# Kernel optimization log

Hardware: AMD Instinct MI355X
Metric: run time of the kernel (lower is better)

Reference implementation:

```python
import jax, jax.numpy as jnp
import numpy as np

D_MODEL = 512

def setup_inputs() -> dict:
    key = jax.random.key(0)
    k1, k2, k3 = jax.random.split(key, 3)
    B, N1, N2 = 16, 2048, 2048
    x1 = jax.random.normal(k1, (B, N1, D_MODEL), dtype=jnp.float32)
    x2 = jax.random.normal(k2, (B, N2, D_MODEL), dtype=jnp.float32)
    node_mask = jnp.ones((B, N1), dtype=jnp.bool_)
    # learned parameter: q_proj weight, stored torch-style [out, in]
    Wq = jax.random.normal(k3, (D_MODEL, D_MODEL), dtype=jnp.float32) * (1.0 / np.sqrt(D_MODEL))
    return {"x1": x1, "x2": x2, "node_mask": node_mask, "Wq": Wq}


def reference(x1, x2, node_mask, Wq):
    # Q = x1 @ Wq^T   (torch Linear with weight [out, in], no bias)
    Q = jnp.einsum('bnd,ed->bne', x1, Wq)            # [B, N1, 512]
    D = x2                                            # [B, N2, 512]
    # similarity matrix L = Q @ D^T
    L = jnp.einsum('bnd,bmd->bnm', Q, D)              # [B, N1, N2]
    # attention over document axis (dim=2)
    A_D = jax.nn.softmax(L, axis=2)                   # [B, N1, N2]
    # C_D = Q^T @ A_D -> transposed to [B, N2, 512]
    C_D = jnp.einsum('bnd,bnm->bmd', Q, A_D)          # [B, N2, 512]
    # attention over query axis (dim=1), then transposed: A_Q [B, N2, N1]
    A_Q = jnp.swapaxes(jax.nn.softmax(L, axis=1), 1, 2)
    # C_Q = D^T @ A_Q -> transposed to [B, N1, 512]
    C_Q = jnp.einsum('bmd,bmn->bnd', D, A_Q)          # [B, N1, 512]
    return (C_Q, C_D, A_D, A_Q)
```

## Files before the change

kernel.cpp:

```cpp
#include <hip/hip_runtime.h>

namespace {

constexpr int Bn = 16;
constexpr int Nn = 2048;
constexpr int Dn = 512;

typedef _Float16 h4 __attribute__((ext_vector_type(4)));
typedef _Float16 h8 __attribute__((ext_vector_type(8)));
typedef float    fx4 __attribute__((ext_vector_type(4)));

__device__ __forceinline__ void gld16(const _Float16* g, _Float16* l) {
  typedef const void __attribute__((address_space(1))) gvoid;
  typedef void __attribute__((address_space(3))) lvoid;
  __builtin_amdgcn_global_load_lds((gvoid*)g, (lvoid*)l, 16, 0, 0);
}

__device__ __forceinline__ void stage_gld(const _Float16* __restrict__ g, int ld,
    int r0, int k0, _Float16* __restrict__ lds, int t)
{
  #pragma unroll
  for (int i = 0; i < 2; ++i) {
    int chunk = i*256 + t;
    gld16(g + (long)(r0 + (chunk >> 2))*ld + k0 + (chunk & 3)*8, lds + chunk*8);
  }
}

__device__ __forceinline__ void load_f32(const float* __restrict__ g, int ld,
    int r0, int k0, int t, fx4* regs)
{
  #pragma unroll
  for (int rd = 0; rd < 4; ++rd)
    regs[rd] = *(const fx4*)(g + (long)(r0 + rd*32 + (t >> 3))*ld + k0 + (t & 7)*4);
}
template<int S>
__device__ __forceinline__ void write_cvt(const fx4* regs, _Float16* __restrict__ lds, int t)
{
  const int c = (t & 7)*4;
  #pragma unroll
  for (int rd = 0; rd < 4; ++rd) {
    int r = rd*32 + (t >> 3);
    h4 o;
    #pragma unroll
    for (int i = 0; i < 4; ++i) o[i] = (_Float16)regs[rd][i];
    *(h4*)(lds + r*S + c) = o;
  }
}

struct RegsA3 { h8 v0, v1; fx4 k00, k01, k10, k11; };
__device__ __forceinline__ void load_A3(const _Float16* __restrict__ g, int ld,
    int r0, int k0, int t, const float* __restrict__ kofs, RegsA3& R)
{
  {
    int chunk = t, r = chunk >> 2, c = (chunk & 3)*8;
    R.v0  = *(const h8*)(g + (long)(r0 + r)*ld + k0 + c);
    R.k00 = *(const fx4*)(kofs + k0 + c);
    R.k01 = *(const fx4*)(kofs + k0 + c + 4);
  }
  {
    int chunk = 256 + t, r = chunk >> 2, c = (chunk & 3)*8;
    R.v1  = *(const h8*)(g + (long)(r0 + r)*ld + k0 + c);
    R.k10 = *(const fx4*)(kofs + k0 + c);
    R.k11 = *(const fx4*)(kofs + k0 + c + 4);
  }
}
template<int S>
__device__ __forceinline__ void write_A3(const RegsA3& R, _Float16* __restrict__ lds, int t)
{
  {
    int chunk = t, r = chunk >> 2, c = (chunk & 3)*8;
    h8 o;
    #pragma unroll
    for (int j = 0; j < 4; ++j) {
      o[j]   = (_Float16)__expf((float)R.v0[j]   - R.k00[j]);
      o[4+j] = (_Float16)__expf((float)R.v0[4+j] - R.k01[j]);
    }
    *(h8*)(lds + r*S + c) = o;
  }
  {
    int chunk = 256 + t, r = chunk >> 2, c = (chunk & 3)*8;
    h8 o;
    #pragma unroll
    for (int j = 0; j < 4; ++j) {
      o[j]   = (_Float16)__expf((float)R.v1[j]   - R.k10[j]);
      o[4+j] = (_Float16)__expf((float)R.v1[4+j] - R.k11[j]);
    }
    *(h8*)(lds + r*S + c) = o;
  }
}

template<int MA, int MB, int EPI, int TY>
__global__ __launch_bounds__(256) void gemm128(
    const void* __restrict__ Ap, long sA,
    const void* __restrict__ Bp, long sB,
    void* __restrict__ Cp, long sC, int ldc,
    void* __restrict__ C2p, long sC2, int ldc2,
    int lda, int ldb, int K,
    const float* __restrict__ kofs,
    float* __restrict__ rowPM, float* __restrict__ rowPS,
    float* __restrict__ colPM, float* __restrict__ colPS)
{
  constexpr int SA = (MA == 0) ? 32 : 40;
  constexpr int SB = (MB == 0) ? 32 : 40;
  constexpr int ASZ = 128*SA, BSZ = 128*SB;
  constexpr int DB = 2*ASZ + 2*BSZ;
  constexpr int SMEM = (EPI >= 1 && DB < 128*136) ? 128*136 : DB;
  __shared__ _Float16 smem[SMEM];

  constexpr int TILES = 16*TY;
  const int bid = blockIdx.x;
  const int xcd = bid & 7, slot = bid >> 3;
  const int b = xcd*2 + slot/TILES;
  const int tile = slot % TILES;
  const int by = tile % TY, bx = tile / TY;
  const int row0 = bx*128, col0 = by*128;

  const int t = threadIdx.x, w = t >> 6, l = t & 63;
  const int wr = w >> 1, wc = w & 1, l15 = l & 15, lg = l >> 4;

  const void* Ab;
  const void* Bb;
  if constexpr (MA == 1) Ab = (const void*)((const float*)Ap + (long)b*sA);
  else                   Ab = (const void*)((const _Float16*)Ap + (long)b*sA);
  if constexpr (MB == 1) Bb = (const void*)((const float*)Bp + (long)b*sB);
  else                   Bb = (const void*)((const _Float16*)Bp + (long)b*sB);

  const float* ko = nullptr;
  if constexpr (MA == 3) ko = kofs + (long)b*Nn;

  fx4 acc[4][4];
  #pragma unroll
  for (int fi = 0; fi < 4; ++fi)
    #pragma unroll
    for (int fj = 0; fj < 4; ++fj)
      acc[fi][fj] = (fx4){0.f, 0.f, 0.f, 0.f};

  const int NT = K/32;
  fx4 regA[4], regB[4];
  RegsA3 rA3;

  if constexpr (MA == 0)      stage_gld((const _Float16*)Ab, lda, row0, 0, smem, t);
  else if constexpr (MA == 1) load_f32((const float*)Ab, lda, row0, 0, t, regA);
  else                        load_A3((const _Float16*)Ab, lda, row0, 0, t, ko, rA3);
  if constexpr (MB == 0)      stage_gld((const _Float16*)Bb, ldb, col0, 0, smem + 2*ASZ, t);
  else                        load_f32((const float*)Bb, ldb, col0, 0, t, regB);
  if constexpr (MA == 1)      write_cvt<SA>(regA, smem, t);
  if constexpr (MA == 3)      write_A3<SA>(rA3, smem, t);
  if constexpr (MB == 1)      write_cvt<SB>(regB, smem + 2*ASZ, t);
  __syncthreads();

  for (int kt = 0; kt < NT; ++kt) {
    const int cur = kt & 1, nxt = cur ^ 1;
    const int k1 = (kt + 1)*32;
    _Float16* cA = smem + cur*ASZ;
    _Float16* cB = smem + 2*ASZ + cur*BSZ;
    _Float16* nA = smem + nxt*ASZ;
    _Float16* nB = smem + 2*ASZ + nxt*BSZ;

    if (kt + 1 < NT) {
      if constexpr (MA == 0)      stage_gld((const _Float16*)Ab, lda, row0, k1, nA, t);
      else if constexpr (MA == 1) load_f32((const float*)Ab, lda, row0, k1, t, regA);
      else                        load_A3((const _Float16*)Ab, lda, row0, k1, t, ko, rA3);
      if constexpr (MB == 0)      stage_gld((const _Float16*)Bb, ldb, col0, k1, nB, t);
      else                        load_f32((const float*)Bb, ldb, col0, k1, t, regB);
    }

    h8 af[4], bf[4];
    #pragma unroll
    for (int fi = 0; fi < 4; ++fi)
      af[fi] = *(const h8*)(cA + (wr*64 + fi*16 + l15)*SA + lg*8);
    #pragma unroll
    for (int fj = 0; fj < 4; ++fj)
      bf[fj] = *(const h8*)(cB + (wc*64 + fj*16 + l15)*SB + lg*8);
    #pragma unroll
    for (int fi = 0; fi < 4; ++fi)
      #pragma unroll
      for (int fj = 0; fj < 4; ++fj)
        acc[fi][fj] = __builtin_amdgcn_mfma_f32_16x16x32_f16(af[fi], bf[fj], acc[fi][fj], 0, 0, 0);

    if (kt + 1 < NT) {
      if constexpr (MA == 1) write_cvt<SA>(regA, nA, t);
      if constexpr (MA == 3) write_A3<SA>(rA3, nA, t);
      if constexpr (MB == 1) write_cvt<SB>(regB, nB, t);
    }
    __syncthreads();
  }

  if constexpr (EPI == 0) {
    float* Cb = (float*)Cp + (long)b*sC;
    #pragma unroll
    for (int fi = 0; fi < 4; ++fi)
      #pragma unroll
      for (int fj = 0; fj < 4; ++fj)
        #pragma unroll
        for (int j = 0; j < 4; ++j)
          Cb[(long)(row0 + wr*64 + fi*16 + lg*4 + j)*ldc + col0 + wc*64 + fj*16 + l15] = acc[fi][fj][j];
  }

  if constexpr (EPI == 1) {
    #pragma unroll
    for (int fi = 0; fi < 4; ++fi)
      #pragma unroll
      for (int fj = 0; fj < 4; ++fj)
        #pragma unroll
        for (int j = 0; j < 4; ++j)
          acc[fi][fj][j] = (float)(_Float16)acc[fi][fj][j];

    #pragma unroll
    for (int fi = 0; fi < 4; ++fi)
      #pragma unroll
      for (int fj = 0; fj < 4; ++fj)
        #pragma unroll
        for (int j = 0; j < 4; ++j)
          smem[(wr*64 + fi*16 + lg*4 + j)*136 + wc*64 + fj*16 + l15] = (_Float16)acc[fi][fj][j];
    __syncthreads();
    _Float16* Cb = (_Float16*)Cp + (long)b*sC;
    #pragma unroll
    for (int rd = 0; rd < 8; ++rd) {
      int r = rd*16 + (t >> 4), c8 = (t & 15)*8;
      h8 v = *(const h8*)(smem + r*136 + c8);
      *(h8*)(Cb + (long)(row0 + r)*ldc + col0 + c8) = v;
    }

    float rm[4][4], rs[4][4];
    #pragma unroll
    for (int fi = 0; fi < 4; ++fi)
      #pragma unroll
      for (int j = 0; j < 4; ++j)
        rm[fi][j] = fmaxf(fmaxf(acc[fi][0][j], acc[fi][1][j]),
                          fmaxf(acc[fi][2][j], acc[fi][3][j]));
    #pragma unroll
    for (int m = 1; m < 16; m <<= 1)
      #pragma unroll
      for (int fi = 0; fi < 4; ++fi)
        #pragma unroll
        for (int j = 0; j < 4; ++j)
          rm[fi][j] = fmaxf(rm[fi][j], __shfl_xor(rm[fi][j], m, 64));
    #pragma unroll
    for (int fi = 0; fi < 4; ++fi)
      #pragma unroll
      for (int j = 0; j < 4; ++j) {
        float s = 0.f;
        #pragma unroll
        for (int fj = 0; fj < 4; ++fj)
          s += __expf(acc[fi][fj][j] - rm[fi][j]);
        rs[fi][j] = s;
      }
    #pragma unroll
    for (int m = 1; m < 16; m <<= 1)
      #pragma unroll
      for (int fi = 0; fi < 4; ++fi)
        #pragma unroll
        for (int j = 0; j < 4; ++j)
          rs[fi][j] += __shfl_xor(rs[fi][j], m, 64);
    if (l15 == 0) {
      #pragma unroll
      for (int fi = 0; fi < 4; ++fi)
        #pragma unroll
        for (int j = 0; j < 4; ++j) {
          int row = row0 + wr*64 + fi*16 + lg*4 + j;
          long idx = ((long)b*Nn + row)*32 + by*2 + wc;
          rowPM[idx] = rm[fi][j];
          rowPS[idx] = rs[fi][j];
        }
    }
    float cm[4], cs[4];
    #pragma unroll
    for (int fj = 0; fj < 4; ++fj) {
      float v = -3.4e38f;
      #pragma unroll
      for (int fi = 0; fi < 4; ++fi)
        #pragma unroll
        for (int j = 0; j < 4; ++j)
          v = fmaxf(v, acc[fi][fj][j]);
      cm[fj] = v;
    }
    #pragma unroll
    for (int fj = 0; fj < 4; ++fj) {
      cm[fj] = fmaxf(cm[fj], __shfl_xor(cm[fj], 16, 64));
      cm[fj] = fmaxf(cm[fj], __shfl_xor(cm[fj], 32, 64));
    }
    #pragma unroll
    for (int fj = 0; fj < 4; ++fj) {
      float s = 0.f;
      #pragma unroll
      for (int fi = 0; fi < 4; ++fi)
        #pragma unroll
        for (int j = 0; j < 4; ++j)
          s += __expf(acc[fi][fj][j] - cm[fj]);
      cs[fj] = s;
    }
    #pragma unroll
    for (int fj = 0; fj < 4; ++fj) {
      cs[fj] += __shfl_xor(cs[fj], 16, 64);
      cs[fj] += __shfl_xor(cs[fj], 32, 64);
    }
    if (l < 16) {
      #pragma unroll
      for (int fj = 0; fj < 4; ++fj) {
        int col = col0 + wc*64 + fj*16 + l15;
        long idx = ((long)b*Nn + col)*32 + bx*2 + wr;
        colPM[idx] = cm[fj];
        colPS[idx] = cs[fj];
      }
    }
  }

  if constexpr (EPI == 2) {
    #pragma unroll
    for (int fi = 0; fi < 4; ++fi)
      #pragma unroll
      for (int fj = 0; fj < 4; ++fj)
        #pragma unroll
        for (int j = 0; j < 4; ++j)
          smem[(wr*64 + fi*16 + lg*4 + j)*136 + wc*64 + fj*16 + l15] = (_Float16)acc[fi][fj][j];
    __syncthreads();
    _Float16* Qb  = (_Float16*)Cp  + (long)b*sC;
    _Float16* QTb = (_Float16*)C2p + (long)b*sC2;
    #pragma unroll
    for (int rd = 0; rd < 8; ++rd) {
      int r = rd*16 + (t >> 4), c8 = (t & 15)*8;
      h8 v = *(const h8*)(smem + r*136 + c8);
      *(h8*)(Qb + (long)(row0 + r)*ldc + col0 + c8) = v;
    }
    #pragma unroll
    for (int rd = 0; rd < 8; ++rd) {
      int dl = rd*16 + (t >> 4), n8 = (t & 15)*8;
      h8 v;
      #pragma unroll
      for (int i = 0; i < 8; ++i) v[i] = smem[(n8 + i)*136 + dl];
      *(h8*)(QTb + (long)(col0 + dl)*ldc2 + row0 + n8) = v;
    }
  }
}

__global__ __launch_bounds__(256) void convert_x2(const float* __restrict__ x2,
    _Float16* __restrict__ x2h, _Float16* __restrict__ x2hT)
{
  __shared__ _Float16 lt[64*66];
  const int b = blockIdx.z, m0 = blockIdx.x*64, d0 = blockIdx.y*64;
  const int t = threadIdx.x;
  const float* xb = x2 + (long)b*Nn*Dn;
  _Float16* hb = x2h + (long)b*Nn*Dn;
  #pragma unroll
  for (int rd = 0; rd < 4; ++rd) {
    int r = rd*16 + (t >> 4), c = (t & 15)*4;
    fx4 v = *(const fx4*)(xb + (long)(m0 + r)*Dn + d0 + c);
    h4 h;
    #pragma unroll
    for (int i = 0; i < 4; ++i) { h[i] = (_Float16)v[i]; lt[r*66 + c + i] = h[i]; }
    *(h4*)(hb + (long)(m0 + r)*Dn + d0 + c) = h;
  }
  __syncthreads();
  _Float16* tb = x2hT + (long)b*Dn*Nn;
  #pragma unroll
  for (int rd = 0; rd < 4; ++rd) {
    int dl = rd*16 + (t >> 4), ml = (t & 15)*4;
    h4 h;
    #pragma unroll
    for (int i = 0; i < 4; ++i) h[i] = lt[(ml + i)*66 + dl];
    *(h4*)(tb + (long)(d0 + dl)*Nn + m0 + ml) = h;
  }
}

__global__ __launch_bounds__(256) void reduce_stats(
    const float* __restrict__ rowPM, const float* __restrict__ rowPS,
    const float* __restrict__ colPM, const float* __restrict__ colPS,
    float* __restrict__ rofs, float* __restrict__ cofs)
{
  const int w = threadIdx.x >> 6, l = threadIdx.x & 63;
  const long row = (long)blockIdx.x*4 + w;
  const float* PM = blockIdx.y ? colPM : rowPM;
  const float* PS = blockIdx.y ? colPS : rowPS;
  float m0 = PM[row*32 + (l & 31)];
  float s0 = PS[row*32 + (l & 31)];
  float m = m0;
  #pragma unroll
  for (int k = 1; k < 32; k <<= 1) m = fmaxf(m, __shfl_xor(m, k, 64));
  float v = s0 * __expf(m0 - m);
  #pragma unroll
  for (int k = 1; k < 32; k <<= 1) v += __shfl_xor(v, k, 64);
  if (l == 0) {
    float ofs = m + __logf(v);
    if (blockIdx.y == 0) rofs[row] = ofs;
    else                 cofs[row] = ofs;
  }
}

__global__ __launch_bounds__(256) void finalize_At(const _Float16* __restrict__ Lh,
    _Float16* __restrict__ At, const float* __restrict__ rofs)
{
  __shared__ _Float16 l1[64*66];
  const int b = blockIdx.z, n0 = blockIdx.x*64, m0 = blockIdx.y*64;
  const int t = threadIdx.x;
  const _Float16* Lb = Lh + (long)b*Nn*Nn;
  #pragma unroll
  for (int rd = 0; rd < 4; ++rd) {
    int r = rd*16 + (t >> 4), c = (t & 15)*4;
    h4 v = *(const h4*)(Lb + (long)(n0 + r)*Nn + m0 + c);
    float ro = rofs[(long)b*Nn + n0 + r];
    #pragma unroll
    for (int i = 0; i < 4; ++i)
      l1[r*66 + c + i] = (_Float16)__expf((float)v[i] - ro);
  }
  __syncthreads();
  _Float16* Ab = At + (long)b*Nn*Nn;
  #pragma unroll
  for (int rd = 0; rd < 4; ++rd) {
    int ml = rd*16 + (t >> 4), nl = (t & 15)*4;
    h4 h;
    #pragma unroll
    for (int i = 0; i < 4; ++i) h[i] = l1[(nl + i)*66 + ml];
    *(h4*)(Ab + (long)(m0 + ml)*Nn + n0 + nl) = h;
  }
}

__global__ __launch_bounds__(256) void finalize_AQ(const _Float16* __restrict__ Lh,
    float* __restrict__ AD, float* __restrict__ AQ,
    const float* __restrict__ rofs, const float* __restrict__ cofs)
{
  __shared__ float l2[64*65];
  const int b = blockIdx.z, n0 = blockIdx.x*64, m0 = blockIdx.y*64;
  const int t = threadIdx.x;
  const _Float16* Lb = Lh + (long)b*Nn*Nn;
  float* Db = AD + (long)b*Nn*Nn;
  #pragma unroll
  for (int rd = 0; rd < 4; ++rd) {
    int r = rd*16 + (t >> 4), c = (t & 15)*4;
    h4 v = *(const h4*)(Lb + (long)(n0 + r)*Nn + m0 + c);
    float ro = rofs[(long)b*Nn + n0 + r];
    fx4 co = *(const fx4*)(cofs + (long)b*Nn + m0 + c);
    fx4 e1;
    #pragma unroll
    for (int i = 0; i < 4; ++i) {
      float lv = (float)v[i];
      e1[i] = __expf(lv - ro);
      l2[r*65 + c + i] = __expf(lv - co[i]);
    }
    *(fx4*)(Db + (long)(n0 + r)*Nn + m0 + c) = e1;
  }
  __syncthreads();
  float* Qb = AQ + (long)b*Nn*Nn;
  #pragma unroll
  for (int rd = 0; rd < 4; ++rd) {
    int ml = rd*16 + (t >> 4), nl = (t & 15)*4;
    fx4 q;
    #pragma unroll
    for (int i = 0; i < 4; ++i) q[i] = l2[(nl + i)*65 + ml];
    *(fx4*)(Qb + (long)(m0 + ml)*Nn + n0 + nl) = q;
  }
}

}

extern "C" void kernel_launch(void* const* d_in, const int* in_sizes, int n_in,
                              void* d_out, int out_size, void* d_ws, size_t ws_size,
                              hipStream_t stream)
{
  const float* x1 = (const float*)d_in[0];
  const float* x2 = (const float*)d_in[1];
  const float* Wq = (const float*)d_in[3];

  float* out = (float*)d_out;
  float* C_Q = out;
  float* C_D = out + (long)Bn*Nn*Dn;
  float* A_D = out + 2L*Bn*Nn*Dn;
  float* A_Q = A_D + (long)Bn*Nn*Nn;

  char* ws = (char*)d_ws;
  _Float16* Qh   = (_Float16*)ws;
  _Float16* QhT  = Qh   + (long)Bn*Nn*Dn;
  _Float16* x2h  = QhT  + (long)Bn*Dn*Nn;
  _Float16* x2hT = x2h  + (long)Bn*Nn*Dn;
  _Float16* Lh   = x2hT + (long)Bn*Dn*Nn;
  float* rofs = (float*)(Lh + (long)Bn*Nn*Nn);
  float* cofs = rofs + (long)Bn*Nn;

  float* rowPM = (float*)A_Q;
  float* rowPS = rowPM + (long)Bn*Nn*32;
  float* colPM = rowPS + (long)Bn*Nn*32;
  float* colPS = colPM + (long)Bn*Nn*32;
  _Float16* At = (_Float16*)A_Q;

  dim3 blk(256);

  convert_x2<<<dim3(32, 8, 16), blk, 0, stream>>>(x2, x2h, x2hT);

  gemm128<1,1,2,4><<<dim3(1024), blk, 0, stream>>>(
      x1, (long)Nn*Dn, Wq, 0L,
      Qh, (long)Nn*Dn, Dn, QhT, (long)Dn*Nn, Nn,
      Dn, Dn, Dn,
      nullptr, nullptr, nullptr, nullptr, nullptr);

  gemm128<0,0,1,16><<<dim3(4096), blk, 0, stream>>>(
      Qh, (long)Nn*Dn, x2h, (long)Nn*Dn,
      Lh, (long)Nn*Nn, Nn, nullptr, 0L, 0,
      Dn, Dn, Dn,
      nullptr, rowPM, rowPS, colPM, colPS);

  reduce_stats<<<dim3(Bn*Nn/4, 2), blk, 0, stream>>>(rowPM, rowPS, colPM, colPS, rofs, cofs);

  gemm128<3,0,0,4><<<dim3(1024), blk, 0, stream>>>(
      Lh, (long)Nn*Nn, x2hT, (long)Dn*Nn,
      C_Q, (long)Nn*Dn, Dn, nullptr, 0L, 0,
      Nn, Nn, Nn,
      cofs, nullptr, nullptr, nullptr, nullptr);

  finalize_At<<<dim3(32, 32, 16), blk, 0, stream>>>(Lh, At, rofs);

  gemm128<0,0,0,4><<<dim3(1024), blk, 0, stream>>>(
      At, (long)Nn*Nn, QhT, (long)Dn*Nn,
      C_D, (long)Nn*Dn, Dn, nullptr, 0L, 0,
      Nn, Nn, Nn,
      nullptr, nullptr, nullptr, nullptr, nullptr);

  finalize_AQ<<<dim3(32, 32, 16), blk, 0, stream>>>(Lh, A_D, A_Q, rofs, cofs);
}
```

Baseline: 624.1 us.

## Emit transposed logits from L GEMM epilogue and drop finalize_At pass

The similarity GEMM epilogue now also writes a transposed fp16 copy of L into scratch inside the A_Q output buffer, using the tile already staged in shared memory. The C_D GEMM then uses its exp-on-load mode (EPI 3) with row offsets on this transposed copy. This removes the separate finalize_At kernel, which read L, exponentiated it and wrote a transposed A. The cost is an extra strided shared-memory gather and a 128 MB global write in the GEMM epilogue, with the partial-stat buffers moved to sit after the transposed copy.

```diff
diff --git a/kernel.cpp b/kernel.cpp
--- a/kernel.cpp
+++ b/kernel.cpp
@@ -214,12 +214,21 @@
         for (int j = 0; j < 4; ++j)
           smem[(wr*64 + fi*16 + lg*4 + j)*136 + wc*64 + fj*16 + l15] = (_Float16)acc[fi][fj][j];
     __syncthreads();
-    _Float16* Cb = (_Float16*)Cp + (long)b*sC;
+    _Float16* LhB = (_Float16*)Cp  + (long)b*sC;
+    _Float16* LtB = (_Float16*)C2p + (long)b*sC2;
     #pragma unroll
     for (int rd = 0; rd < 8; ++rd) {
       int r = rd*16 + (t >> 4), c8 = (t & 15)*8;
       h8 v = *(const h8*)(smem + r*136 + c8);
-      *(h8*)(Cb + (long)(row0 + r)*ldc + col0 + c8) = v;
+      *(h8*)(LhB + (long)(row0 + r)*ldc + col0 + c8) = v;
+    }
+    #pragma unroll
+    for (int rd = 0; rd < 8; ++rd) {
+      int dl = rd*16 + (t >> 4), n8 = (t & 15)*8;
+      h8 v;
+      #pragma unroll
+      for (int i = 0; i < 8; ++i) v[i] = smem[(n8 + i)*136 + dl];
+      *(h8*)(LtB + (long)(col0 + dl)*ldc2 + row0 + n8) = v;
     }
 
     float rm[4][4], rs[4][4];
@@ -384,34 +393,6 @@
     float ofs = m + __logf(v);
     if (blockIdx.y == 0) rofs[row] = ofs;
     else                 cofs[row] = ofs;
-  }
-}
-
-__global__ __launch_bounds__(256) void finalize_At(const _Float16* __restrict__ Lh,
-    _Float16* __restrict__ At, const float* __restrict__ rofs)
-{
-  __shared__ _Float16 l1[64*66];
-  const int b = blockIdx.z, n0 = blockIdx.x*64, m0 = blockIdx.y*64;
-  const int t = threadIdx.x;
-  const _Float16* Lb = Lh + (long)b*Nn*Nn;
-  #pragma unroll
-  for (int rd = 0; rd < 4; ++rd) {
-    int r = rd*16 + (t >> 4), c = (t & 15)*4;
-    h4 v = *(const h4*)(Lb + (long)(n0 + r)*Nn + m0 + c);
-    float ro = rofs[(long)b*Nn + n0 + r];
-    #pragma unroll
-    for (int i = 0; i < 4; ++i)
-      l1[r*66 + c + i] = (_Float16)__expf((float)v[i] - ro);
-  }
-  __syncthreads();
-  _Float16* Ab = At + (long)b*Nn*Nn;
-  #pragma unroll
-  for (int rd = 0; rd < 4; ++rd) {
-    int ml = rd*16 + (t >> 4), nl = (t & 15)*4;
-    h4 h;
-    #pragma unroll
-    for (int i = 0; i < 4; ++i) h[i] = l1[(nl + i)*66 + ml];
-    *(h4*)(Ab + (long)(m0 + ml)*Nn + n0 + nl) = h;
   }
 }
 
@@ -476,11 +457,11 @@
   float* rofs = (float*)(Lh + (long)Bn*Nn*Nn);
   float* cofs = rofs + (long)Bn*Nn;
 
-  float* rowPM = (float*)A_Q;
+  _Float16* Lt = (_Float16*)A_Q;
+  float* rowPM = (float*)((char*)A_Q + sizeof(_Float16)*(long)Bn*Nn*Nn);
   float* rowPS = rowPM + (long)Bn*Nn*32;
   float* colPM = rowPS + (long)Bn*Nn*32;
   float* colPS = colPM + (long)Bn*Nn*32;
-  _Float16* At = (_Float16*)A_Q;
 
   dim3 blk(256);
 
@@ -494,7 +475,7 @@
 
   gemm128<0,0,1,16><<<dim3(4096), blk, 0, stream>>>(
       Qh, (long)Nn*Dn, x2h, (long)Nn*Dn,
-      Lh, (long)Nn*Nn, Nn, nullptr, 0L, 0,
+      Lh, (long)Nn*Nn, Nn, Lt, (long)Nn*Nn, Nn,
       Dn, Dn, Dn,
       nullptr, rowPM, rowPS, colPM, colPS);
 
@@ -506,13 +487,11 @@
       Nn, Nn, Nn,
       cofs, nullptr, nullptr, nullptr, nullptr);
 
-  finalize_At<<<dim3(32, 32, 16), blk, 0, stream>>>(Lh, At, rofs);
-
-  gemm128<0,0,0,4><<<dim3(1024), blk, 0, stream>>>(
-      At, (long)Nn*Nn, QhT, (long)Dn*Nn,
+  gemm128<3,0,0,4><<<dim3(1024), blk, 0, stream>>>(
+      Lt, (long)Nn*Nn, QhT, (long)Dn*Nn,
       C_D, (long)Nn*Dn, Dn, nullptr, 0L, 0,
       Nn, Nn, Nn,
-      nullptr, nullptr, nullptr, nullptr, nullptr);
+      rofs, nullptr, nullptr, nullptr, nullptr);
 
   finalize_AQ<<<dim3(32, 32, 16), blk, 0, stream>>>(Lh, A_D, A_Q, rofs, cofs);
 }
```

Result: slower. 679.6 us (+8.9%).
